# Performance work log

Measured on AMD Instinct MI355X. Metric: run time of the kernel, lower is better.

Reference implementation:

```python
import jax, jax.numpy as jnp
import numpy as np

N_NODES = 100000
N_EDGES = 1600000
N_GRAPHS = 128
BEHAVIOR_DIM = 32
LLM_DIM = 768
LLM_PROJ = 32
HIDDEN = 64
NUM_CLASSES = 2
INPUT_DIM = 64 + 16 + LLM_PROJ + BEHAVIOR_DIM  # 144


def gcn_conv(h, edge_index, edge_weight, W, b, n):
    """PyG GCNConv: linear -> gcn_norm with self-loops -> scatter-add at target."""
    h = h @ W  # [N, out]
    row, col = edge_index[0], edge_index[1]
    loop = jnp.arange(n)
    row_f = jnp.concatenate([row, loop])
    col_f = jnp.concatenate([col, loop])
    ew_f = jnp.concatenate([edge_weight, jnp.ones((n,), h.dtype)])
    deg = jax.ops.segment_sum(ew_f, col_f, num_segments=n)
    dinv = jnp.where(deg > 0, jax.lax.rsqrt(deg), 0.0)
    norm = dinv[row_f] * ew_f * dinv[col_f]  # [E+N]
    out = jax.ops.segment_sum(norm[:, None] * h[row_f], col_f, num_segments=n)
    return out + b


def global_mean_pool(x, batch, num_graphs):
    s = jax.ops.segment_sum(x, batch, num_segments=num_graphs)
    cnt = jax.ops.segment_sum(jnp.ones((x.shape[0],), x.dtype), batch, num_segments=num_graphs)
    return s / jnp.maximum(cnt, 1.0)[:, None]


def setup_inputs() -> dict:
    key = jax.random.key(0)
    ks = jax.random.split(key, 16)
    inp = {
        "x_names": jax.random.randint(ks[0], (N_NODES,), 0, 20000),
        "x_types": jax.random.randint(ks[1], (N_NODES,), 0, 100),
        "x_behaviors": jax.random.normal(ks[2], (N_NODES, BEHAVIOR_DIM), jnp.float32),
        "edge_index": jax.random.randint(ks[3], (2, N_EDGES), 0, N_NODES),
        "edge_weight": jax.random.uniform(ks[4], (N_EDGES,), jnp.float32),
        "batch": jnp.sort(jax.random.randint(ks[5], (N_NODES,), 0, N_GRAPHS)),
        "llm_features": jax.random.normal(ks[6], (N_NODES, LLM_DIM), jnp.float32),
        # parameters
        "name_emb": jax.random.normal(ks[7], (20000, 64), jnp.float32),
        "type_emb": jax.random.normal(ks[8], (100, 16), jnp.float32),
        "llm_proj_w": jax.random.normal(ks[9], (LLM_DIM, LLM_PROJ), jnp.float32) * 0.02,
        "llm_proj_b": jnp.zeros((LLM_PROJ,), jnp.float32),
        "conv1_w": jax.random.normal(ks[10], (INPUT_DIM, HIDDEN), jnp.float32) * 0.08,
        "conv1_b": jnp.zeros((HIDDEN,), jnp.float32),
        "conv2_w": jax.random.normal(ks[11], (HIDDEN, HIDDEN), jnp.float32) * 0.12,
        "conv2_b": jnp.zeros((HIDDEN,), jnp.float32),
        "cls_w": jax.random.normal(ks[12], (HIDDEN, NUM_CLASSES), jnp.float32) * 0.12,
        "cls_b": jnp.zeros((NUM_CLASSES,), jnp.float32),
    }
    return inp


def reference(x_names, x_types, x_behaviors, edge_index, edge_weight, batch,
              llm_features, name_emb, type_emb, llm_proj_w, llm_proj_b,
              conv1_w, conv1_b, conv2_w, conv2_b, cls_w, cls_b):
    n = x_names.shape[0]
    name_feat = name_emb[x_names]          # [N, 64]
    type_feat = type_emb[x_types]          # [N, 16]
    llm_feat = llm_features @ llm_proj_w + llm_proj_b  # [N, 32]
    x = jnp.concatenate([name_feat, type_feat, llm_feat, x_behaviors], axis=1)
    # dropout is identity in eval mode
    x = jax.nn.relu(gcn_conv(x, edge_index, edge_weight, conv1_w, conv1_b, n))
    x = jax.nn.relu(gcn_conv(x, edge_index, edge_weight, conv2_w, conv2_b, n))
    x = global_mean_pool(x, batch, N_GRAPHS)  # [G, HIDDEN]
    return x @ cls_w + cls_b                   # [G, 2]
```

## Files before the change

kernel.cpp:

```cpp
#include <hip/hip_runtime.h>
#include <cstdint>
#include <cstddef>

typedef __attribute__((ext_vector_type(8))) _Float16 f16x8;
typedef __attribute__((ext_vector_type(4))) _Float16 f16x4;
typedef __attribute__((ext_vector_type(4))) float f32x4;

__device__ __forceinline__ f16x8 cvt8(const float4& p, const float4& q) {
  f16x8 r;
  r[0] = (_Float16)p.x; r[1] = (_Float16)p.y; r[2] = (_Float16)p.z; r[3] = (_Float16)p.w;
  r[4] = (_Float16)q.x; r[5] = (_Float16)q.y; r[6] = (_Float16)q.z; r[7] = (_Float16)q.w;
  return r;
}


__global__ void prep_kernel(const float* __restrict__ pw, const float* __restrict__ pb,
                            const float* __restrict__ w1, const float* __restrict__ w2,
                            _Float16* __restrict__ Bf, float* __restrict__ biasf,
                            _Float16* __restrict__ B2f) {
  int idx = blockIdx.x * 256 + threadIdx.x;
  if (idx < 896 * 64) {
    int gk = idx >> 6, col = idx & 63;
    float val;
    if (gk < 768) {
      float acc = 0.0f;
      #pragma unroll 8
      for (int m = 0; m < 32; ++m) acc = fmaf(pw[gk * 32 + m], w1[(80 + m) * 64 + col], acc);
      val = acc;
    } else if (gk < 832) val = w1[(gk - 768) * 64 + col];
    else if (gk < 848)   val = w1[(64 + gk - 832) * 64 + col];
    else if (gk < 864)   val = w1[(112 + gk - 848) * 64 + col];
    else if (gk < 880)   val = w1[(128 + gk - 864) * 64 + col];
    else                 val = 0.0f;
    int chunk = gk >> 5, k = gk & 31;
    int g, j;
    if (k < 16) { g = k >> 2; j = k & 3; } else { int k2 = k - 16; g = k2 >> 2; j = 4 + (k2 & 3); }
    Bf[((size_t)(chunk * 4 + g) * 64 + col) * 8 + j] = (_Float16)val;
  } else if (idx < 896 * 64 + 64) {
    int col = idx - 896 * 64;
    float acc = 0.0f;
    for (int m = 0; m < 32; ++m) acc = fmaf(pb[m], w1[(80 + m) * 64 + col], acc);
    biasf[col] = acc;
  } else if (idx < 896 * 64 + 64 + 64 * 64) {
    int q2 = idx - (896 * 64 + 64);
    int gk = q2 >> 6, col = q2 & 63;
    float val = w2[gk * 64 + col];
    int chunk = gk >> 5, k = gk & 31;
    int g, j;
    if (k < 16) { g = k >> 2; j = k & 3; } else { int k2 = k - 16; g = k2 >> 2; j = 4 + (k2 & 3); }
    B2f[((size_t)(chunk * 4 + g) * 64 + col) * 8 + j] = (_Float16)val;
  }
}


__global__ void cnt_kernel(const int* __restrict__ ei, int* __restrict__ cnt, int E) {
  int e = blockIdx.x * 256 + threadIdx.x;
  if (e < E) atomicAdd(&cnt[ei[E + e]], 1);
}

__global__ __launch_bounds__(256) void scan_blk(const int* __restrict__ cnt,
                                                int* __restrict__ colp,
                                                int* __restrict__ bsum, int n) {
  __shared__ int ws[4];
  int t = threadIdx.x, lane = t & 63, w = t >> 6;
  int i = blockIdx.x * 256 + t;
  int v = (i < n) ? cnt[i] : 0;
  int x = v;
  #pragma unroll
  for (int off = 1; off < 64; off <<= 1) { int y = __shfl_up(x, off); if (lane >= off) x += y; }
  if (lane == 63) ws[w] = x;
  __syncthreads();
  if (t == 0) {
    int s = 0;
    #pragma unroll
    for (int k = 0; k < 4; ++k) { int tmp = ws[k]; ws[k] = s; s += tmp; }
    bsum[blockIdx.x] = s;
  }
  __syncthreads();
  if (i < n) colp[i] = ws[w] + x - v;
}

__global__ __launch_bounds__(512) void scan_top(int* __restrict__ bsum,
                                                int* __restrict__ colp, int nb, int n) {
  __shared__ int ws[8];
  int t = threadIdx.x, lane = t & 63, w = t >> 6;
  int v = (t < nb) ? bsum[t] : 0;
  int x = v;
  #pragma unroll
  for (int off = 1; off < 64; off <<= 1) { int y = __shfl_up(x, off); if (lane >= off) x += y; }
  if (lane == 63) ws[w] = x;
  __syncthreads();
  if (t == 0) {
    int s = 0;
    #pragma unroll
    for (int k = 0; k < 8; ++k) { int tmp = ws[k]; ws[k] = s; s += tmp; }
  }
  __syncthreads();
  int excl = ws[w] + x - v;
  if (t < nb) bsum[t] = excl;
  if (t == nb - 1) colp[n] = excl + v;
}

__global__ void scan_add(int* __restrict__ colp, int* __restrict__ fillp,
                         const int* __restrict__ bsum, int n) {
  int i = blockIdx.x * 256 + threadIdx.x;
  if (i < n) {
    int c = colp[i] + bsum[blockIdx.x];
    colp[i] = c;
    fillp[i] = c;
  }
}

__global__ void fill_kernel(const int* __restrict__ ei, const float* __restrict__ ew,
                            int* __restrict__ fillp, int2* __restrict__ csr, int E) {
  int e = blockIdx.x * 256 + threadIdx.x;
  if (e >= E) return;
  int row = ei[e], col = ei[E + e];
  int pos = atomicAdd(&fillp[col], 1);
  csr[pos] = make_int2(row, __float_as_int(ew[e]));
}

__global__ void degsum_kernel(const int* __restrict__ colp, const int2* __restrict__ csr,
                              float* __restrict__ dinv, int n) {
  int j = blockIdx.x * 256 + threadIdx.x;
  if (j >= n) return;
  int e0 = colp[j], e1 = colp[j + 1];
  float s = 1.0f;
  for (int e = e0; e < e1; ++e) s += __int_as_float(csr[e].y);
  dinv[j] = rsqrtf(s);
}


__device__ __forceinline__ void loadBf(const _Float16* __restrict__ Bf, int c, int g, int r16,
                                       f16x8 (&bf)[4]) {
  #pragma unroll
  for (int ct = 0; ct < 4; ++ct)
    bf[ct] = *(const f16x8*)(Bf + ((size_t)(c * 4 + g) * 64 + ct * 16 + r16) * 8);
}

__device__ __forceinline__ void mfma8(f32x4 (&acc)[2][4], const f16x8& a0, const f16x8& a1,
                                      const f16x8 (&bf)[4]) {
  #pragma unroll
  for (int ct = 0; ct < 4; ++ct) {
    acc[0][ct] = __builtin_amdgcn_mfma_f32_16x16x32_f16(a0, bf[ct], acc[0][ct], 0, 0, 0);
    acc[1][ct] = __builtin_amdgcn_mfma_f32_16x16x32_f16(a1, bf[ct], acc[1][ct], 0, 0, 0);
  }
}

__global__ __launch_bounds__(256, 3) void gemm1_kernel(
    const float* __restrict__ llm, const _Float16* __restrict__ Bf,
    const int* __restrict__ names, const int* __restrict__ types,
    const float* __restrict__ beh, const float* __restrict__ nemb,
    const float* __restrict__ temb, const float* __restrict__ biasf,
    const float* __restrict__ dinv, _Float16* __restrict__ out, int n)
{
  int nwg = gridDim.x;
  int b = blockIdx.x;
  int q = nwg >> 3, r = nwg & 7;
  int xcd = b & 7, bidx = b >> 3;
  int swz = (xcd < r ? xcd * (q + 1) : r * (q + 1) + (xcd - r) * q) + bidx;

  int w = swz * 4 + (threadIdx.x >> 6);
  int nw = (n + 31) >> 5;
  if (w >= nw) return;
  int lane = threadIdx.x & 63;
  int g = lane >> 4, r16 = lane & 15;
  int base = w * 32;

  int arow0 = base + r16;      if (arow0 > n - 1) arow0 = n - 1;
  int arow1 = base + 16 + r16; if (arow1 > n - 1) arow1 = n - 1;
  int nm0 = names[arow0], nm1 = names[arow1];
  int tp0 = types[arow0], tp1 = types[arow1];

  const float* pA0 = llm + (size_t)arow0 * 768 + g * 4;
  const float* pA1 = llm + (size_t)arow1 * 768 + g * 4;

  f32x4 acc[2][4];
  #pragma unroll
  for (int i = 0; i < 2; ++i)
    #pragma unroll
    for (int j = 0; j < 4; ++j) { acc[i][j][0] = 0.f; acc[i][j][1] = 0.f; acc[i][j][2] = 0.f; acc[i][j][3] = 0.f; }

  float4 X0l = *(const float4*)(pA0 +  0), X0h = *(const float4*)(pA0 + 16);
  float4 X1l = *(const float4*)(pA1 +  0), X1h = *(const float4*)(pA1 + 16);
  float4 Y0l = *(const float4*)(pA0 + 32), Y0h = *(const float4*)(pA0 + 48);
  float4 Y1l = *(const float4*)(pA1 + 32), Y1h = *(const float4*)(pA1 + 48);
  float4 Z0l = *(const float4*)(pA0 + 64), Z0h = *(const float4*)(pA0 + 80);
  float4 Z1l = *(const float4*)(pA1 + 64), Z1h = *(const float4*)(pA1 + 80);

  f16x8 bf[4], a0, a1;

  #pragma unroll 1
  for (int cc = 0; cc < 7; ++cc) {
    const int c = cc * 3;
    loadBf(Bf, c, g, r16, bf);
    a0 = cvt8(X0l, X0h); a1 = cvt8(X1l, X1h);
    X0l = *(const float4*)(pA0 + (c + 3) * 32);
    X0h = *(const float4*)(pA0 + (c + 3) * 32 + 16);
    X1l = *(const float4*)(pA1 + (c + 3) * 32);
    X1h = *(const float4*)(pA1 + (c + 3) * 32 + 16);
    __builtin_amdgcn_sched_barrier(0);
    mfma8(acc, a0, a1, bf);
    loadBf(Bf, c + 1, g, r16, bf);
    a0 = cvt8(Y0l, Y0h); a1 = cvt8(Y1l, Y1h);
    Y0l = *(const float4*)(pA0 + (c + 4) * 32);
    Y0h = *(const float4*)(pA0 + (c + 4) * 32 + 16);
    Y1l = *(const float4*)(pA1 + (c + 4) * 32);
    Y1h = *(const float4*)(pA1 + (c + 4) * 32 + 16);
    __builtin_amdgcn_sched_barrier(0);
    mfma8(acc, a0, a1, bf);
    loadBf(Bf, c + 2, g, r16, bf);
    a0 = cvt8(Z0l, Z0h); a1 = cvt8(Z1l, Z1h);
    Z0l = *(const float4*)(pA0 + (c + 5) * 32);
    Z0h = *(const float4*)(pA0 + (c + 5) * 32 + 16);
    Z1l = *(const float4*)(pA1 + (c + 5) * 32);
    Z1h = *(const float4*)(pA1 + (c + 5) * 32 + 16);
    __builtin_amdgcn_sched_barrier(0);
    mfma8(acc, a0, a1, bf);
  }

  loadBf(Bf, 21, g, r16, bf);
  a0 = cvt8(X0l, X0h); a1 = cvt8(X1l, X1h);
  mfma8(acc, a0, a1, bf);
  loadBf(Bf, 22, g, r16, bf);
  a0 = cvt8(Y0l, Y0h); a1 = cvt8(Y1l, Y1h);
  mfma8(acc, a0, a1, bf);
  loadBf(Bf, 23, g, r16, bf);
  a0 = cvt8(Z0l, Z0h); a1 = cvt8(Z1l, Z1h);
  mfma8(acc, a0, a1, bf);

  const float* pN0 = nemb + (size_t)nm0 * 64 + g * 4;
  const float* pN1 = nemb + (size_t)nm1 * 64 + g * 4;
  #pragma unroll
  for (int t = 0; t < 2; ++t) {
    float4 l0 = *(const float4*)(pN0 + t * 32), h0 = *(const float4*)(pN0 + t * 32 + 16);
    float4 l1 = *(const float4*)(pN1 + t * 32), h1 = *(const float4*)(pN1 + t * 32 + 16);
    loadBf(Bf, 24 + t, g, r16, bf);
    a0 = cvt8(l0, h0); a1 = cvt8(l1, h1);
    mfma8(acc, a0, a1, bf);
  }
  {
    float4 l0 = *(const float4*)(temb + (size_t)tp0 * 16 + g * 4);
    float4 h0 = *(const float4*)(beh + (size_t)arow0 * 32 + g * 4);
    float4 l1 = *(const float4*)(temb + (size_t)tp1 * 16 + g * 4);
    float4 h1 = *(const float4*)(beh + (size_t)arow1 * 32 + g * 4);
    loadBf(Bf, 26, g, r16, bf);
    a0 = cvt8(l0, h0); a1 = cvt8(l1, h1);
    mfma8(acc, a0, a1, bf);
  }
  {
    const float4 z = make_float4(0.f, 0.f, 0.f, 0.f);
    float4 l0 = *(const float4*)(beh + (size_t)arow0 * 32 + 16 + g * 4);
    float4 l1 = *(const float4*)(beh + (size_t)arow1 * 32 + 16 + g * 4);
    loadBf(Bf, 27, g, r16, bf);
    a0 = cvt8(l0, z); a1 = cvt8(l1, z);
    mfma8(acc, a0, a1, bf);
  }

  float dv0[4], dv1[4];
  #pragma unroll
  for (int rr = 0; rr < 4; ++rr) {
    int n0 = base + g * 4 + rr;      dv0[rr] = dinv[n0 < n ? n0 : n - 1];
    int n1 = base + 16 + g * 4 + rr; dv1[rr] = dinv[n1 < n ? n1 : n - 1];
  }
  #pragma unroll
  for (int ct = 0; ct < 4; ++ct) {
    int col = ct * 16 + r16;
    float bfc = biasf[col];
    #pragma unroll
    for (int rr = 0; rr < 4; ++rr) {
      int node0 = base + g * 4 + rr;
      if (node0 < n) out[(size_t)node0 * 64 + col] = (_Float16)((acc[0][ct][rr] + bfc) * dv0[rr]);
      int node1 = base + 16 + g * 4 + rr;
      if (node1 < n) out[(size_t)node1 * 64 + col] = (_Float16)((acc[1][ct][rr] + bfc) * dv1[rr]);
    }
  }
}


__global__ __launch_bounds__(256, 4) void gemm2_kernel(
    const _Float16* __restrict__ h, const _Float16* __restrict__ B2f,
    const float* __restrict__ dinv, _Float16* __restrict__ out, int n)
{
  int w = blockIdx.x * 4 + (threadIdx.x >> 6);
  int nw = (n + 31) >> 5;
  if (w >= nw) return;
  int lane = threadIdx.x & 63;
  int g = lane >> 4, r16 = lane & 15;
  int base = w * 32;
  int arow0 = base + r16;      if (arow0 > n - 1) arow0 = n - 1;
  int arow1 = base + 16 + r16; if (arow1 > n - 1) arow1 = n - 1;

  f32x4 acc[2][4];
  #pragma unroll
  for (int i = 0; i < 2; ++i)
    #pragma unroll
    for (int j = 0; j < 4; ++j) { acc[i][j][0] = 0.f; acc[i][j][1] = 0.f; acc[i][j][2] = 0.f; acc[i][j][3] = 0.f; }

  #pragma unroll
  for (int c = 0; c < 2; ++c) {
    f16x8 bf[4];
    loadBf(B2f, c, g, r16, bf);
    const _Float16* p0 = h + (size_t)arow0 * 64 + c * 32 + g * 4;
    const _Float16* p1 = h + (size_t)arow1 * 64 + c * 32 + g * 4;
    f16x4 lo0 = *(const f16x4*)p0, hi0 = *(const f16x4*)(p0 + 16);
    f16x4 lo1 = *(const f16x4*)p1, hi1 = *(const f16x4*)(p1 + 16);
    f16x8 a0, a1;
    a0[0] = lo0[0]; a0[1] = lo0[1]; a0[2] = lo0[2]; a0[3] = lo0[3];
    a0[4] = hi0[0]; a0[5] = hi0[1]; a0[6] = hi0[2]; a0[7] = hi0[3];
    a1[0] = lo1[0]; a1[1] = lo1[1]; a1[2] = lo1[2]; a1[3] = lo1[3];
    a1[4] = hi1[0]; a1[5] = hi1[1]; a1[6] = hi1[2]; a1[7] = hi1[3];
    mfma8(acc, a0, a1, bf);
  }

  float dv0[4], dv1[4];
  #pragma unroll
  for (int rr = 0; rr < 4; ++rr) {
    int n0 = base + g * 4 + rr;      dv0[rr] = dinv[n0 < n ? n0 : n - 1];
    int n1 = base + 16 + g * 4 + rr; dv1[rr] = dinv[n1 < n ? n1 : n - 1];
  }
  #pragma unroll
  for (int ct = 0; ct < 4; ++ct) {
    int col = ct * 16 + r16;
    #pragma unroll
    for (int rr = 0; rr < 4; ++rr) {
      int node0 = base + g * 4 + rr;
      if (node0 < n) out[(size_t)node0 * 64 + col] = (_Float16)(acc[0][ct][rr] * dv0[rr]);
      int node1 = base + 16 + g * 4 + rr;
      if (node1 < n) out[(size_t)node1 * 64 + col] = (_Float16)(acc[1][ct][rr] * dv1[rr]);
    }
  }
}


template <typename OUT>
__global__ __launch_bounds__(256) void agg_kernel(
    const _Float16* __restrict__ hp, const int* __restrict__ colp,
    const int2* __restrict__ csr, const float* __restrict__ dinv,
    const float* __restrict__ bias, OUT* __restrict__ out, int n)
{
  int wid = threadIdx.x >> 6, lane = threadIdx.x & 63;
  int j = blockIdx.x * 4 + wid;
  if (j >= n) return;
  float dj = dinv[j];
  float hj = (float)hp[(size_t)j * 64 + lane];
  int e0 = colp[j], e1 = colp[j + 1];
  float s0 = 0.0f, s1 = 0.0f;
  int e = e0;
  for (; e + 8 <= e1; e += 8) {
    int2 m0 = csr[e],     m1 = csr[e + 1], m2 = csr[e + 2], m3 = csr[e + 3];
    int2 m4 = csr[e + 4], m5 = csr[e + 5], m6 = csr[e + 6], m7 = csr[e + 7];
    float f0 = (float)hp[(size_t)m0.x * 64 + lane];
    float f1 = (float)hp[(size_t)m1.x * 64 + lane];
    float f2 = (float)hp[(size_t)m2.x * 64 + lane];
    float f3 = (float)hp[(size_t)m3.x * 64 + lane];
    float f4 = (float)hp[(size_t)m4.x * 64 + lane];
    float f5 = (float)hp[(size_t)m5.x * 64 + lane];
    float f6 = (float)hp[(size_t)m6.x * 64 + lane];
    float f7 = (float)hp[(size_t)m7.x * 64 + lane];
    s0 = fmaf(__int_as_float(m0.y), f0, s0);
    s1 = fmaf(__int_as_float(m1.y), f1, s1);
    s0 = fmaf(__int_as_float(m2.y), f2, s0);
    s1 = fmaf(__int_as_float(m3.y), f3, s1);
    s0 = fmaf(__int_as_float(m4.y), f4, s0);
    s1 = fmaf(__int_as_float(m5.y), f5, s1);
    s0 = fmaf(__int_as_float(m6.y), f6, s0);
    s1 = fmaf(__int_as_float(m7.y), f7, s1);
  }
  for (; e + 2 <= e1; e += 2) {
    int2 m0 = csr[e], m1 = csr[e + 1];
    float f0 = (float)hp[(size_t)m0.x * 64 + lane];
    float f1 = (float)hp[(size_t)m1.x * 64 + lane];
    s0 = fmaf(__int_as_float(m0.y), f0, s0);
    s1 = fmaf(__int_as_float(m1.y), f1, s1);
  }
  if (e < e1) {
    int2 m = csr[e];
    s0 = fmaf(__int_as_float(m.y), (float)hp[(size_t)m.x * 64 + lane], s0);
  }
  float acc = bias[lane] + dj * (hj + s0 + s1);
  out[(size_t)j * 64 + lane] = (OUT)fmaxf(acc, 0.0f);
}


__global__ __launch_bounds__(256) void pool_kernel(const float* __restrict__ x,
                                                   const int* __restrict__ batch,
                                                   float* __restrict__ pooled, int n) {
  __shared__ float red[4][64];
  __shared__ int range_s[2];
  int gph = blockIdx.x;
  int tid = threadIdx.x, wid = tid >> 6, lane = tid & 63;
  if (tid < 2) {
    int target = gph + tid;
    int lo = 0, hi = n;
    while (lo < hi) { int m = (lo + hi) >> 1; if (batch[m] < target) lo = m + 1; else hi = m; }
    range_s[tid] = lo;
  }
  __syncthreads();
  int lo = range_s[0], hi = range_s[1];
  float acc = 0.0f;
  for (int i = lo + wid; i < hi; i += 4) acc += x[(size_t)i * 64 + lane];
  red[wid][lane] = acc;
  __syncthreads();
  if (tid < 64) {
    float sum = red[0][lane] + red[1][lane] + red[2][lane] + red[3][lane];
    float cntf = (float)(hi - lo);
    pooled[gph * 64 + lane] = sum / fmaxf(cntf, 1.0f);
  }
}

__global__ void cls_kernel(const float* __restrict__ pooled, const float* __restrict__ cw,
                           const float* __restrict__ cb, float* __restrict__ out) {
  int t = threadIdx.x;
  int gph = t >> 1, c = t & 1;
  float acc = cb[c];
  #pragma unroll 8
  for (int k = 0; k < 64; ++k) acc = fmaf(pooled[gph * 64 + k], cw[k * 2 + c], acc);
  out[gph * 2 + c] = acc;
}


extern "C" void kernel_launch(void* const* d_in, const int* in_sizes, int n_in,
                              void* d_out, int out_size, void* d_ws, size_t ws_size,
                              hipStream_t stream) {
  const int*   x_names  = (const int*)  d_in[0];
  const int*   x_types  = (const int*)  d_in[1];
  const float* behav    = (const float*)d_in[2];
  const int*   ei       = (const int*)  d_in[3];
  const float* ew       = (const float*)d_in[4];
  const int*   batch    = (const int*)  d_in[5];
  const float* llm      = (const float*)d_in[6];
  const float* name_emb = (const float*)d_in[7];
  const float* type_emb = (const float*)d_in[8];
  const float* pw       = (const float*)d_in[9];
  const float* pb       = (const float*)d_in[10];
  const float* w1       = (const float*)d_in[11];
  const float* b1       = (const float*)d_in[12];
  const float* w2       = (const float*)d_in[13];
  const float* b2       = (const float*)d_in[14];
  const float* cw       = (const float*)d_in[15];
  const float* cb       = (const float*)d_in[16];

  const int N = in_sizes[0];
  const int E = in_sizes[4];
  const int nb = (N + 255) / 256;
  const int eb = (E + 255) / 256;
  const int gblocks = ((N + 31) / 32 + 3) / 4;

  char* p = (char*)d_ws;
  auto alloc = [&](size_t bytes) -> void* {
    void* r = (void*)p; p += (bytes + 255) & ~(size_t)255; return r;
  };
  float*     dinv   = (float*)    alloc((size_t)N * 4);
  int*       cnt    = (int*)      alloc((size_t)N * 4);
  int*       colp   = (int*)      alloc((size_t)(N + 1) * 4);
  int*       fillp  = (int*)      alloc((size_t)N * 4);
  int2*      csr    = (int2*)     alloc((size_t)E * 8);
  int*       bsum   = (int*)      alloc((size_t)(nb + 1) * 4);
  _Float16*  Bf     = (_Float16*) alloc((size_t)896 * 64 * 2);
  _Float16*  B2f    = (_Float16*) alloc((size_t)64 * 64 * 2);
  float*     biasf  = (float*)    alloc((size_t)64 * 4);
  _Float16*  hp1    = (_Float16*) alloc((size_t)N * 64 * 2);
  _Float16*  y1     = (_Float16*) alloc((size_t)N * 64 * 2);
  _Float16*  hp2    = (_Float16*) alloc((size_t)N * 64 * 2);
  float*     y2     = (float*)    alloc((size_t)N * 64 * 4);
  float*     pooled = (float*)    alloc((size_t)128 * 64 * 4);
  (void)ws_size; (void)n_in; (void)out_size;

  prep_kernel<<<(896 * 64 + 64 + 64 * 64 + 255) / 256, 256, 0, stream>>>(
      pw, pb, w1, w2, Bf, biasf, B2f);
  hipMemsetAsync(cnt, 0, (size_t)N * 4, stream);
  cnt_kernel<<<eb, 256, 0, stream>>>(ei, cnt, E);
  scan_blk<<<nb, 256, 0, stream>>>(cnt, colp, bsum, N);
  scan_top<<<1, 512, 0, stream>>>(bsum, colp, nb, N);
  scan_add<<<nb, 256, 0, stream>>>(colp, fillp, bsum, N);
  fill_kernel<<<eb, 256, 0, stream>>>(ei, ew, fillp, csr, E);
  degsum_kernel<<<nb, 256, 0, stream>>>(colp, csr, dinv, N);

  gemm1_kernel<<<gblocks, 256, 0, stream>>>(llm, Bf, x_names, x_types, behav,
                                            name_emb, type_emb, biasf, dinv, hp1, N);
  agg_kernel<_Float16><<<(N + 3) / 4, 256, 0, stream>>>(hp1, colp, csr, dinv, b1, y1, N);
  gemm2_kernel<<<gblocks, 256, 0, stream>>>(y1, B2f, dinv, hp2, N);
  agg_kernel<float><<<(N + 3) / 4, 256, 0, stream>>>(hp2, colp, csr, dinv, b2, y2, N);
  pool_kernel<<<128, 256, 0, stream>>>(y2, batch, pooled, N);
  cls_kernel<<<1, 256, 0, stream>>>(pooled, cw, cb, (float*)d_out);
}
```

Before: 479.8 us.

## Widen gemm loads to contiguous 16-float chunks and fold memset into prep

Reorders the packed weight layout so each lane group reads 16 contiguous floats of the LLM/embedding rows per 64-wide K step, replacing the strided 4+4 float pattern with wider contiguous loads. The gemm2 A-operand becomes a single 16-byte f16x8 load. The count memset moves into the prep kernel, and the separate fill-pointer array is dropped by running the fill atomics on colp directly, which shifts the offsets by one so readers use colp[j-1] and colp[j]. This trims a memset launch, a copy pass and some load instructions, at the cost of a more intricate K-permutation that must match between prep and the gemm kernels.

```diff
diff --git a/kernel.cpp b/kernel.cpp
--- a/kernel.cpp
+++ b/kernel.cpp
@@ -17,8 +17,9 @@
 __global__ void prep_kernel(const float* __restrict__ pw, const float* __restrict__ pb,
                             const float* __restrict__ w1, const float* __restrict__ w2,
                             _Float16* __restrict__ Bf, float* __restrict__ biasf,
-                            _Float16* __restrict__ B2f) {
+                            _Float16* __restrict__ B2f, int* __restrict__ cnt, int n) {
   int idx = blockIdx.x * 256 + threadIdx.x;
+  if (idx < n) cnt[idx] = 0;
   if (idx < 896 * 64) {
     int gk = idx >> 6, col = idx & 63;
     float val;
@@ -29,13 +30,11 @@
       val = acc;
     } else if (gk < 832) val = w1[(gk - 768) * 64 + col];
     else if (gk < 848)   val = w1[(64 + gk - 832) * 64 + col];
-    else if (gk < 864)   val = w1[(112 + gk - 848) * 64 + col];
-    else if (gk < 880)   val = w1[(128 + gk - 864) * 64 + col];
+    else if (gk < 880)   val = w1[(112 + gk - 848) * 64 + col];
     else                 val = 0.0f;
-    int chunk = gk >> 5, k = gk & 31;
-    int g, j;
-    if (k < 16) { g = k >> 2; j = k & 3; } else { int k2 = k - 16; g = k2 >> 2; j = 4 + (k2 & 3); }
-    Bf[((size_t)(chunk * 4 + g) * 64 + col) * 8 + j] = (_Float16)val;
+    int step = gk >> 6, kk = gk & 63;
+    int g = kk >> 4, half = (kk >> 3) & 1, j = kk & 7;
+    Bf[(((size_t)(step * 2 + half) * 4 + g) * 64 + col) * 8 + j] = (_Float16)val;
   } else if (idx < 896 * 64 + 64) {
     int col = idx - 896 * 64;
     float acc = 0.0f;
@@ -46,8 +45,7 @@
     int gk = q2 >> 6, col = q2 & 63;
     float val = w2[gk * 64 + col];
     int chunk = gk >> 5, k = gk & 31;
-    int g, j;
-    if (k < 16) { g = k >> 2; j = k & 3; } else { int k2 = k - 16; g = k2 >> 2; j = 4 + (k2 & 3); }
+    int g = k >> 3, j = k & 7;
     B2f[((size_t)(chunk * 4 + g) * 64 + col) * 8 + j] = (_Float16)val;
   }
 }
@@ -101,22 +99,17 @@
   if (t == nb - 1) colp[n] = excl + v;
 }
 
-__global__ void scan_add(int* __restrict__ colp, int* __restrict__ fillp,
-                         const int* __restrict__ bsum, int n) {
+__global__ void scan_add(int* __restrict__ colp, const int* __restrict__ bsum, int n) {
   int i = blockIdx.x * 256 + threadIdx.x;
-  if (i < n) {
-    int c = colp[i] + bsum[blockIdx.x];
-    colp[i] = c;
-    fillp[i] = c;
-  }
+  if (i < n) colp[i] += bsum[blockIdx.x];
 }
 
 __global__ void fill_kernel(const int* __restrict__ ei, const float* __restrict__ ew,
-                            int* __restrict__ fillp, int2* __restrict__ csr, int E) {
+                            int* __restrict__ colp, int2* __restrict__ csr, int E) {
   int e = blockIdx.x * 256 + threadIdx.x;
   if (e >= E) return;
   int row = ei[e], col = ei[E + e];
-  int pos = atomicAdd(&fillp[col], 1);
+  int pos = atomicAdd(&colp[col], 1);
   csr[pos] = make_int2(row, __float_as_int(ew[e]));
 }
 
@@ -124,7 +117,8 @@
                               float* __restrict__ dinv, int n) {
   int j = blockIdx.x * 256 + threadIdx.x;
   if (j >= n) return;
-  int e0 = colp[j], e1 = colp[j + 1];
+  int e0 = (j > 0) ? colp[j - 1] : 0;
+  int e1 = colp[j];
   float s = 1.0f;
   for (int e = e0; e < e1; ++e) s += __int_as_float(csr[e].y);
   dinv[j] = rsqrtf(s);
@@ -172,8 +166,8 @@
   int nm0 = names[arow0], nm1 = names[arow1];
   int tp0 = types[arow0], tp1 = types[arow1];
 
-  const float* pA0 = llm + (size_t)arow0 * 768 + g * 4;
-  const float* pA1 = llm + (size_t)arow1 * 768 + g * 4;
+  const float* pA0 = llm + (size_t)arow0 * 768 + g * 16;
+  const float* pA1 = llm + (size_t)arow1 * 768 + g * 16;
 
   f32x4 acc[2][4];
   #pragma unroll
@@ -181,80 +175,89 @@
     #pragma unroll
     for (int j = 0; j < 4; ++j) { acc[i][j][0] = 0.f; acc[i][j][1] = 0.f; acc[i][j][2] = 0.f; acc[i][j][3] = 0.f; }
 
-  float4 X0l = *(const float4*)(pA0 +  0), X0h = *(const float4*)(pA0 + 16);
-  float4 X1l = *(const float4*)(pA1 +  0), X1h = *(const float4*)(pA1 + 16);
-  float4 Y0l = *(const float4*)(pA0 + 32), Y0h = *(const float4*)(pA0 + 48);
-  float4 Y1l = *(const float4*)(pA1 + 32), Y1h = *(const float4*)(pA1 + 48);
-  float4 Z0l = *(const float4*)(pA0 + 64), Z0h = *(const float4*)(pA0 + 80);
-  float4 Z1l = *(const float4*)(pA1 + 64), Z1h = *(const float4*)(pA1 + 80);
-
-  f16x8 bf[4], a0, a1;
+  float4 X[8], Y[8];
+  #pragma unroll
+  for (int t = 0; t < 4; ++t) {
+    X[t]     = *(const float4*)(pA0 + t * 4);
+    X[4 + t] = *(const float4*)(pA1 + t * 4);
+    Y[t]     = *(const float4*)(pA0 + 64 + t * 4);
+    Y[4 + t] = *(const float4*)(pA1 + 64 + t * 4);
+  }
+
+  f16x8 bf[4], a0, a1, o0, o1;
 
   #pragma unroll 1
-  for (int cc = 0; cc < 7; ++cc) {
-    const int c = cc * 3;
-    loadBf(Bf, c, g, r16, bf);
-    a0 = cvt8(X0l, X0h); a1 = cvt8(X1l, X1h);
-    X0l = *(const float4*)(pA0 + (c + 3) * 32);
-    X0h = *(const float4*)(pA0 + (c + 3) * 32 + 16);
-    X1l = *(const float4*)(pA1 + (c + 3) * 32);
-    X1h = *(const float4*)(pA1 + (c + 3) * 32 + 16);
+  for (int ss = 0; ss < 5; ++ss) {
+    const int s = ss * 2;
+    loadBf(Bf, s * 2, g, r16, bf);
+    a0 = cvt8(X[0], X[1]); a1 = cvt8(X[4], X[5]);
+    o0 = cvt8(X[2], X[3]); o1 = cvt8(X[6], X[7]);
+    #pragma unroll
+    for (int t = 0; t < 4; ++t) {
+      X[t]     = *(const float4*)(pA0 + (s + 2) * 64 + t * 4);
+      X[4 + t] = *(const float4*)(pA1 + (s + 2) * 64 + t * 4);
+    }
     __builtin_amdgcn_sched_barrier(0);
     mfma8(acc, a0, a1, bf);
-    loadBf(Bf, c + 1, g, r16, bf);
-    a0 = cvt8(Y0l, Y0h); a1 = cvt8(Y1l, Y1h);
-    Y0l = *(const float4*)(pA0 + (c + 4) * 32);
-    Y0h = *(const float4*)(pA0 + (c + 4) * 32 + 16);
-    Y1l = *(const float4*)(pA1 + (c + 4) * 32);
-    Y1h = *(const float4*)(pA1 + (c + 4) * 32 + 16);
+    loadBf(Bf, s * 2 + 1, g, r16, bf);
+    mfma8(acc, o0, o1, bf);
+    loadBf(Bf, (s + 1) * 2, g, r16, bf);
+    a0 = cvt8(Y[0], Y[1]); a1 = cvt8(Y[4], Y[5]);
+    o0 = cvt8(Y[2], Y[3]); o1 = cvt8(Y[6], Y[7]);
+    #pragma unroll
+    for (int t = 0; t < 4; ++t) {
+      Y[t]     = *(const float4*)(pA0 + (s + 3) * 64 + t * 4);
+      Y[4 + t] = *(const float4*)(pA1 + (s + 3) * 64 + t * 4);
+    }
     __builtin_amdgcn_sched_barrier(0);
     mfma8(acc, a0, a1, bf);
-    loadBf(Bf, c + 2, g, r16, bf);
-    a0 = cvt8(Z0l, Z0h); a1 = cvt8(Z1l, Z1h);
-    Z0l = *(const float4*)(pA0 + (c + 5) * 32);
-    Z0h = *(const float4*)(pA0 + (c + 5) * 32 + 16);
-    Z1l = *(const float4*)(pA1 + (c + 5) * 32);
-    Z1h = *(const float4*)(pA1 + (c + 5) * 32 + 16);
-    __builtin_amdgcn_sched_barrier(0);
-    mfma8(acc, a0, a1, bf);
-  }
-
+    loadBf(Bf, (s + 1) * 2 + 1, g, r16, bf);
+    mfma8(acc, o0, o1, bf);
+  }
+
+  loadBf(Bf, 20, g, r16, bf);
+  a0 = cvt8(X[0], X[1]); a1 = cvt8(X[4], X[5]);
+  o0 = cvt8(X[2], X[3]); o1 = cvt8(X[6], X[7]);
+  mfma8(acc, a0, a1, bf);
   loadBf(Bf, 21, g, r16, bf);
-  a0 = cvt8(X0l, X0h); a1 = cvt8(X1l, X1h);
-  mfma8(acc, a0, a1, bf);
+  mfma8(acc, o0, o1, bf);
+
   loadBf(Bf, 22, g, r16, bf);
-  a0 = cvt8(Y0l, Y0h); a1 = cvt8(Y1l, Y1h);
+  a0 = cvt8(Y[0], Y[1]); a1 = cvt8(Y[4], Y[5]);
+  o0 = cvt8(Y[2], Y[3]); o1 = cvt8(Y[6], Y[7]);
   mfma8(acc, a0, a1, bf);
   loadBf(Bf, 23, g, r16, bf);
-  a0 = cvt8(Z0l, Z0h); a1 = cvt8(Z1l, Z1h);
-  mfma8(acc, a0, a1, bf);
-
-  const float* pN0 = nemb + (size_t)nm0 * 64 + g * 4;
-  const float* pN1 = nemb + (size_t)nm1 * 64 + g * 4;
-  #pragma unroll
-  for (int t = 0; t < 2; ++t) {
-    float4 l0 = *(const float4*)(pN0 + t * 32), h0 = *(const float4*)(pN0 + t * 32 + 16);
-    float4 l1 = *(const float4*)(pN1 + t * 32), h1 = *(const float4*)(pN1 + t * 32 + 16);
-    loadBf(Bf, 24 + t, g, r16, bf);
-    a0 = cvt8(l0, h0); a1 = cvt8(l1, h1);
+  mfma8(acc, o0, o1, bf);
+
+  {
+    const float* pN0 = nemb + (size_t)nm0 * 64 + g * 16;
+    const float* pN1 = nemb + (size_t)nm1 * 64 + g * 16;
+    float4 u[8];
+    #pragma unroll
+    for (int t = 0; t < 4; ++t) { u[t] = *(const float4*)(pN0 + t * 4); u[4 + t] = *(const float4*)(pN1 + t * 4); }
+    loadBf(Bf, 24, g, r16, bf);
+    a0 = cvt8(u[0], u[1]); a1 = cvt8(u[4], u[5]);
+    o0 = cvt8(u[2], u[3]); o1 = cvt8(u[6], u[7]);
     mfma8(acc, a0, a1, bf);
-  }
-  {
-    float4 l0 = *(const float4*)(temb + (size_t)tp0 * 16 + g * 4);
-    float4 h0 = *(const float4*)(beh + (size_t)arow0 * 32 + g * 4);
-    float4 l1 = *(const float4*)(temb + (size_t)tp1 * 16 + g * 4);
-    float4 h1 = *(const float4*)(beh + (size_t)arow1 * 32 + g * 4);
-    loadBf(Bf, 26, g, r16, bf);
-    a0 = cvt8(l0, h0); a1 = cvt8(l1, h1);
-    mfma8(acc, a0, a1, bf);
+    loadBf(Bf, 25, g, r16, bf);
+    mfma8(acc, o0, o1, bf);
   }
   {
     const float4 z = make_float4(0.f, 0.f, 0.f, 0.f);
-    float4 l0 = *(const float4*)(beh + (size_t)arow0 * 32 + 16 + g * 4);
-    float4 l1 = *(const float4*)(beh + (size_t)arow1 * 32 + 16 + g * 4);
+    const float* q0 = (g == 0) ? (temb + (size_t)tp0 * 16)
+                               : (beh + (size_t)arow0 * 32 + (size_t)((g - 1) & 1) * 16);
+    const float* q1 = (g == 0) ? (temb + (size_t)tp1 * 16)
+                               : (beh + (size_t)arow1 * 32 + (size_t)((g - 1) & 1) * 16);
+    float4 u[8];
+    #pragma unroll
+    for (int t = 0; t < 4; ++t) { u[t] = *(const float4*)(q0 + t * 4); u[4 + t] = *(const float4*)(q1 + t * 4); }
+    if (g == 3) { u[0] = z; u[1] = z; u[2] = z; u[3] = z; u[4] = z; u[5] = z; u[6] = z; u[7] = z; }
+    loadBf(Bf, 26, g, r16, bf);
+    a0 = cvt8(u[0], u[1]); a1 = cvt8(u[4], u[5]);
+    o0 = cvt8(u[2], u[3]); o1 = cvt8(u[6], u[7]);
+    mfma8(acc, a0, a1, bf);
     loadBf(Bf, 27, g, r16, bf);
-    a0 = cvt8(l0, z); a1 = cvt8(l1, z);
-    mfma8(acc, a0, a1, bf);
+    mfma8(acc, o0, o1, bf);
   }
 
   float dv0[4], dv1[4];
@@ -301,15 +304,8 @@
   for (int c = 0; c < 2; ++c) {
     f16x8 bf[4];
     loadBf(B2f, c, g, r16, bf);
-    const _Float16* p0 = h + (size_t)arow0 * 64 + c * 32 + g * 4;
-    const _Float16* p1 = h + (size_t)arow1 * 64 + c * 32 + g * 4;
-    f16x4 lo0 = *(const f16x4*)p0, hi0 = *(const f16x4*)(p0 + 16);
-    f16x4 lo1 = *(const f16x4*)p1, hi1 = *(const f16x4*)(p1 + 16);
-    f16x8 a0, a1;
-    a0[0] = lo0[0]; a0[1] = lo0[1]; a0[2] = lo0[2]; a0[3] = lo0[3];
-    a0[4] = hi0[0]; a0[5] = hi0[1]; a0[6] = hi0[2]; a0[7] = hi0[3];
-    a1[0] = lo1[0]; a1[1] = lo1[1]; a1[2] = lo1[2]; a1[3] = lo1[3];
-    a1[4] = hi1[0]; a1[5] = hi1[1]; a1[6] = hi1[2]; a1[7] = hi1[3];
+    f16x8 a0 = *(const f16x8*)(h + (size_t)arow0 * 64 + c * 32 + g * 8);
+    f16x8 a1 = *(const f16x8*)(h + (size_t)arow1 * 64 + c * 32 + g * 8);
     mfma8(acc, a0, a1, bf);
   }
 
@@ -344,7 +340,8 @@
   if (j >= n) return;
   float dj = dinv[j];
   float hj = (float)hp[(size_t)j * 64 + lane];
-  int e0 = colp[j], e1 = colp[j + 1];
+  int e0 = (j > 0) ? colp[j - 1] : 0;
+  int e1 = colp[j];
   float s0 = 0.0f, s1 = 0.0f;
   int e = e0;
   for (; e + 8 <= e1; e += 8) {
@@ -454,7 +451,6 @@
   float*     dinv   = (float*)    alloc((size_t)N * 4);
   int*       cnt    = (int*)      alloc((size_t)N * 4);
   int*       colp   = (int*)      alloc((size_t)(N + 1) * 4);
-  int*       fillp  = (int*)      alloc((size_t)N * 4);
   int2*      csr    = (int2*)     alloc((size_t)E * 8);
   int*       bsum   = (int*)      alloc((size_t)(nb + 1) * 4);
   _Float16*  Bf     = (_Float16*) alloc((size_t)896 * 64 * 2);
@@ -467,14 +463,14 @@
   float*     pooled = (float*)    alloc((size_t)128 * 64 * 4);
   (void)ws_size; (void)n_in; (void)out_size;
 
-  prep_kernel<<<(896 * 64 + 64 + 64 * 64 + 255) / 256, 256, 0, stream>>>(
-      pw, pb, w1, w2, Bf, biasf, B2f);
-  hipMemsetAsync(cnt, 0, (size_t)N * 4, stream);
+  int prep_blocks = (896 * 64 + 64 + 64 * 64 + 255) / 256;
+  if (prep_blocks < nb) prep_blocks = nb;
+  prep_kernel<<<prep_blocks, 256, 0, stream>>>(pw, pb, w1, w2, Bf, biasf, B2f, cnt, N);
   cnt_kernel<<<eb, 256, 0, stream>>>(ei, cnt, E);
   scan_blk<<<nb, 256, 0, stream>>>(cnt, colp, bsum, N);
   scan_top<<<1, 512, 0, stream>>>(bsum, colp, nb, N);
-  scan_add<<<nb, 256, 0, stream>>>(colp, fillp, bsum, N);
-  fill_kernel<<<eb, 256, 0, stream>>>(ei, ew, fillp, csr, E);
+  scan_add<<<nb, 256, 0, stream>>>(colp, bsum, N);
+  fill_kernel<<<eb, 256, 0, stream>>>(ei, ew, colp, csr, E);
   degsum_kernel<<<nb, 256, 0, stream>>>(colp, csr, dinv, N);
 
   gemm1_kernel<<<gblocks, 256, 0, stream>>>(llm, Bf, x_names, x_types, behav,
```

New measurement: 593.9 us. +23.8%, slower.
